# Kernel tuning notes

Hardware: AMD Instinct MI355X
Metric: run time of the kernel (lower is better)

Reference implementation:

```python
import jax, jax.numpy as jnp
import numpy as np

SCALE = 2.0 ** 10.5
DROPOUT_P = 0.5


def setup_inputs() -> dict:
    key = jax.random.key(0)
    ks = jax.random.split(key, 8)
    B, G, S, D_IN, D_H = 1, 8, 4096, 3, 8
    return {
        "x1": jax.random.normal(ks[0], (B, G, S, D_IN), dtype=jnp.float32),
        "x2": jax.random.normal(ks[1], (B, G, S, D_IN), dtype=jnp.float32),
        "Wq": jax.random.normal(ks[2], (D_H, D_IN), dtype=jnp.float32),
        "bq": jax.random.normal(ks[3], (D_H,), dtype=jnp.float32),
        "Wk": jax.random.normal(ks[4], (D_H, D_IN), dtype=jnp.float32),
        "bk": jax.random.normal(ks[5], (D_H,), dtype=jnp.float32),
        "Wv": jax.random.normal(ks[6], (D_H, D_IN), dtype=jnp.float32),
        "bv": jax.random.normal(ks[7], (D_H,), dtype=jnp.float32),
    }


def reference(x1, x2, Wq, bq, Wk, bk, Wv, bv):
    # Linear projections (torch Linear: x @ W.T + b)
    q = jnp.einsum("bgsd,hd->bgsh", x1, Wq) + bq  # [B,G,S,8]
    k = jnp.einsum("bgsd,hd->bgsh", x2, Wk) + bk
    v = jnp.einsum("bgsd,hd->bgsh", x1, Wv) + bv
    # scores scaled by custom factor 2**10.5 (multiplied, not divided)
    scores = jnp.einsum("bgsh,bgth->bgst", q, k) * jnp.float32(SCALE)  # [B,G,S,S]
    probs = jax.nn.softmax(scores, axis=-1)
    # dropout p=0.5 (training mode), deterministic mask, inverted scaling
    mask = jax.random.bernoulli(jax.random.key(42), 1.0 - DROPOUT_P, probs.shape)
    probs = jnp.where(mask, probs / jnp.float32(1.0 - DROPOUT_P), jnp.float32(0.0))
    out = jnp.einsum("bgst,bgth->bgsh", probs, v)  # [B,G,S,8]
    return out
```

## Files before the change

kernel.cpp:

```cpp
#include <hip/hip_runtime.h>
#include <stdint.h>

namespace {

constexpr int G = 8;
constexpr int S = 4096;
constexpr int RPB = 64;
constexpr int RPW = 8;
constexpr int NW = 8;
constexpr int LOGCAP = 64;
constexpr float K2C = (float)(1448.15468787004945 * 1.44269504088896340736);
constexpr float CUT = 32.0f;

__device__ __forceinline__ uint32_t rotl32(uint32_t x, uint32_t n) {
  return (x << n) | (x >> (32u - n));
}

__device__ __forceinline__ void tfround(uint32_t& x0, uint32_t& x1, uint32_t r) {
  x0 += x1;
  x1 = rotl32(x1, r);
  x1 ^= x0;
}

__device__ __forceinline__ void threefry2x32(uint32_t c0, uint32_t c1,
                                             uint32_t& r0, uint32_t& r1) {
  const uint32_t ks0 = 0u;
  const uint32_t ks1 = 42u;
  const uint32_t ks2 = 0x1BD11BF0u;
  uint32_t x0 = c0 + ks0;
  uint32_t x1 = c1 + ks1;
  tfround(x0, x1, 13); tfround(x0, x1, 15); tfround(x0, x1, 26); tfround(x0, x1, 6);
  x0 += ks1; x1 += ks2 + 1u;
  tfround(x0, x1, 17); tfround(x0, x1, 29); tfround(x0, x1, 16); tfround(x0, x1, 24);
  x0 += ks2; x1 += ks0 + 2u;
  tfround(x0, x1, 13); tfround(x0, x1, 15); tfround(x0, x1, 26); tfround(x0, x1, 6);
  x0 += ks0; x1 += ks1 + 3u;
  tfround(x0, x1, 17); tfround(x0, x1, 29); tfround(x0, x1, 16); tfround(x0, x1, 24);
  x0 += ks1; x1 += ks2 + 4u;
  tfround(x0, x1, 13); tfround(x0, x1, 15); tfround(x0, x1, 26); tfround(x0, x1, 6);
  x0 += ks2; x1 += ks0 + 5u;
  r0 = x0; r1 = x1;
}

__device__ __forceinline__ bool keep_mask(uint32_t i) {
  uint32_t a, b;
  threefry2x32(0u, i, a, b);
  return (((a ^ b) >> 31) == 0u);
}

__global__ __launch_bounds__(512, 4)
void fused_attn(const float* __restrict__ x1, const float* __restrict__ x2,
                const float* __restrict__ Wq, const float* __restrict__ bq,
                const float* __restrict__ Wk, const float* __restrict__ bk,
                const float* __restrict__ Wv, const float* __restrict__ bv,
                float* __restrict__ out) {
  __shared__ __align__(16) float XS[S];
  __shared__ __align__(16) float YS[S];
  __shared__ __align__(16) float ZS[S];
  __shared__ float4 CKs[RPB];
  __shared__ uint32_t LOGB[NW][LOGCAP * 2];

  const int g = blockIdx.x >> 6;
  const int tile = blockIdx.x & 63;
  const int row0 = tile * RPB;
  const int tid = (int)threadIdx.x;
  const int wave = tid >> 6;
  const int lane = tid & 63;

  const float* x2g = x2 + (size_t)g * S * 3;
  const float* x1g = x1 + (size_t)g * S * 3;

  if (tid < RPB) {
    const float* px = x1g + (size_t)(row0 + tid) * 3;
    const float a0 = px[0], a1 = px[1], a2 = px[2];
    float q[8];
#pragma unroll
    for (int h = 0; h < 8; ++h)
      q[h] = bq[h] + a0 * Wq[h * 3 + 0] + a1 * Wq[h * 3 + 1] + a2 * Wq[h * 3 + 2];
    float t0 = 0.f, t1 = 0.f, t2 = 0.f, t3 = 0.f;
#pragma unroll
    for (int h = 0; h < 8; ++h) {
      t0 += q[h] * Wk[h * 3 + 0];
      t1 += q[h] * Wk[h * 3 + 1];
      t2 += q[h] * Wk[h * 3 + 2];
      t3 += q[h] * bk[h];
    }
    CKs[tid] = make_float4(t0 * K2C, t1 * K2C, t2 * K2C, t3 * K2C);
  }

  {
    const float4* src = (const float4*)x2g;
    float4* X4 = (float4*)XS;
    float4* Y4 = (float4*)YS;
    float4* Z4 = (float4*)ZS;
    float4 tmp[6];
#pragma unroll
    for (int it = 0; it < 2; ++it)
#pragma unroll
      for (int k = 0; k < 3; ++k)
        tmp[it * 3 + k] = src[it * 1536 + tid * 3 + k];
#pragma unroll
    for (int it = 0; it < 2; ++it) {
      const float4 f0 = tmp[it * 3 + 0];
      const float4 f1 = tmp[it * 3 + 1];
      const float4 f2 = tmp[it * 3 + 2];
      const int gi = it * 512 + tid;
      X4[gi] = make_float4(f0.x, f0.w, f1.z, f2.y);
      Y4[gi] = make_float4(f0.y, f1.x, f1.w, f2.z);
      Z4[gi] = make_float4(f0.z, f1.y, f2.x, f2.w);
    }
  }
  __syncthreads();

  const float4* X4 = (const float4*)XS;
  const float4* Y4 = (const float4*)YS;
  const float4* Z4 = (const float4*)ZS;

  float4 CK[RPW];
#pragma unroll
  for (int r = 0; r < RPW; ++r) CK[r] = CKs[wave * RPW + r];

  float m[RPW];
#pragma unroll
  for (int r = 0; r < RPW; ++r) m[r] = -3.0e38f;

#pragma unroll 2
  for (int c = 0; c < S / 4 / 64; ++c) {
    const int i4 = (c << 6) + lane;
    const float4 fx = X4[i4], fy = Y4[i4], fz = Z4[i4];
    const float bxa[4] = {fx.x, fx.y, fx.z, fx.w};
    const float bya[4] = {fy.x, fy.y, fy.z, fy.w};
    const float bza[4] = {fz.x, fz.y, fz.z, fz.w};
#pragma unroll
    for (int e = 0; e < 4; ++e) {
      const float bx = bxa[e], by = bya[e], bz = bza[e];
#pragma unroll
      for (int r = 0; r < RPW; ++r)
        m[r] = fmaxf(m[r], fmaf(CK[r].x, bx,
                     fmaf(CK[r].y, by, fmaf(CK[r].z, bz, CK[r].w))));
    }
  }
#pragma unroll
  for (int msk = 1; msk < 64; msk <<= 1) {
#pragma unroll
    for (int r = 0; r < RPW; ++r) m[r] = fmaxf(m[r], __shfl_xor(m[r], msk, 64));
  }
#pragma unroll
  for (int r = 0; r < RPW; ++r) CK[r].w -= m[r];

  uint32_t* LOG = LOGB[wave];
  int cnt = 0;

#pragma unroll 2
  for (int c = 0; c < S / 4 / 64; ++c) {
    const int i4 = (c << 6) + lane;
    const float4 fx = X4[i4], fy = Y4[i4], fz = Z4[i4];
    const float bxa[4] = {fx.x, fx.y, fx.z, fx.w};
    const float bya[4] = {fy.x, fy.y, fy.z, fy.w};
    const float bza[4] = {fz.x, fz.y, fz.z, fz.w};
#pragma unroll
    for (int e = 0; e < 4; ++e) {
      const float bx = bxa[e], by = bya[e], bz = bza[e];
      float d[RPW];
#pragma unroll
      for (int r = 0; r < RPW; ++r)
        d[r] = fmaf(CK[r].x, bx, fmaf(CK[r].y, by, fmaf(CK[r].z, bz, CK[r].w)));
      const float m01 = fmaxf(fmaxf(d[0], d[1]), fmaxf(d[2], d[3]));
      const float m23 = fmaxf(fmaxf(d[4], d[5]), fmaxf(d[6], d[7]));
      const float mx = fmaxf(m01, m23);
      if (__any(mx > -CUT)) {
        const uint32_t tt = (uint32_t)((i4 << 2) + e);
#pragma unroll
        for (int r = 0; r < RPW; ++r) {
          const bool hit = (d[r] > -CUT);
          const unsigned long long bm = __ballot(hit);
          if (bm) {
            const int pos = cnt + (int)__popcll(bm & ((1ull << lane) - 1ull));
            if (hit && pos < LOGCAP) {
              LOG[pos * 2 + 0] = ((uint32_t)r << 12) | tt;
              LOG[pos * 2 + 1] = __float_as_uint(d[r]);
            }
            cnt += (int)__popcll(bm);
          }
        }
      }
    }
  }
  if (cnt > LOGCAP) cnt = LOGCAP;

  const uint32_t grow0 = (uint32_t)(g * S + row0 + wave * RPW);
  float lr = 0.f, lkp = 0.f, a0 = 0.f, a1 = 0.f, a2 = 0.f;

  for (int base = 0; base < cnt; base += 64) {
    const int idx = base + lane;
    const bool val = (idx < cnt);
    const uint32_t w0 = val ? LOG[idx * 2 + 0] : 0u;
    const float dd = val ? __uint_as_float(LOG[idx * 2 + 1]) : 0.0f;
    const int er = (int)(w0 >> 12);
    const uint32_t et = w0 & 4095u;
    const float pr = val ? exp2f(dd) : 0.0f;
    const bool keep = val && keep_mask(((grow0 + (uint32_t)er) << 12) | et);
    float c0 = 0.f, c1 = 0.f, c2 = 0.f, prk = 0.f;
    if (keep) {
      const float* pa = x1g + 3u * et;
      prk = pr;
      c0 = pr * pa[0]; c1 = pr * pa[1]; c2 = pr * pa[2];
    }
    const int nj = (cnt - base < 64) ? (cnt - base) : 64;
    for (int jj = 0; jj < nj; ++jj) {
      const int rj = __shfl(er, jj, 64);
      const float prj = __shfl(pr, jj, 64);
      const float prkj = __shfl(prk, jj, 64);
      const float c0j = __shfl(c0, jj, 64);
      const float c1j = __shfl(c1, jj, 64);
      const float c2j = __shfl(c2, jj, 64);
      const bool mine = (rj == lane);
      lr += mine ? prj : 0.f;
      lkp += mine ? prkj : 0.f;
      a0 += mine ? c0j : 0.f;
      a1 += mine ? c1j : 0.f;
      a2 += mine ? c2j : 0.f;
    }
  }

  if (lane < RPW) {
    const int srow = row0 + wave * RPW + lane;
    const float sc = 2.0f / lr;
    float o[8];
#pragma unroll
    for (int h = 0; h < 8; ++h)
      o[h] = (bv[h] * lkp + Wv[h * 3 + 0] * a0 + Wv[h * 3 + 1] * a1 +
              Wv[h * 3 + 2] * a2) * sc;
    float4* po = (float4*)(out + (size_t)(g * S + srow) * 8);
    po[0] = make_float4(o[0], o[1], o[2], o[3]);
    po[1] = make_float4(o[4], o[5], o[6], o[7]);
  }
}

}

extern "C" void kernel_launch(void* const* d_in, const int* in_sizes, int n_in,
                              void* d_out, int out_size, void* d_ws, size_t ws_size,
                              hipStream_t stream) {
  (void)in_sizes; (void)n_in; (void)d_ws; (void)ws_size; (void)out_size;
  const float* x1 = (const float*)d_in[0];
  const float* x2 = (const float*)d_in[1];
  const float* Wq = (const float*)d_in[2];
  const float* bq = (const float*)d_in[3];
  const float* Wk = (const float*)d_in[4];
  const float* bk = (const float*)d_in[5];
  const float* Wv = (const float*)d_in[6];
  const float* bv = (const float*)d_in[7];
  float* out = (float*)d_out;

  fused_attn<<<dim3(G * (S / RPB)), dim3(512), 0, stream>>>(
      x1, x2, Wq, bq, Wk, bk, Wv, bv, out);
}
```

Before: 91.02 us.

## Replace full max pass with seeded partial max and online rescaling

Instead of a full pass over all 4096 keys to compute each row's exact max, the kernel seeds the max from the first 512 keys, then logs candidates above a threshold relative to that seed and tracks the true max of logged entries for rescaling during accumulation. This removes one of the two full score sweeps. In exchange, the log capacity grows to 256 entries per wave, stored as uint2. Because the seed max can underestimate the true max, more entries may pass the cutoff and overflow the log, which risks dropped terms. The accumulate loop's selects are also rewritten as FMAs with a 0/1 factor.

```diff
diff --git a/kernel.cpp b/kernel.cpp
--- a/kernel.cpp
+++ b/kernel.cpp
@@ -8,7 +8,8 @@
 constexpr int RPB = 64;
 constexpr int RPW = 8;
 constexpr int NW = 8;
-constexpr int LOGCAP = 64;
+constexpr int LOGCAP = 256;
+constexpr int SEEDC = 2;
 constexpr float K2C = (float)(1448.15468787004945 * 1.44269504088896340736);
 constexpr float CUT = 32.0f;
 
@@ -58,7 +59,7 @@
   __shared__ __align__(16) float YS[S];
   __shared__ __align__(16) float ZS[S];
   __shared__ float4 CKs[RPB];
-  __shared__ uint32_t LOGB[NW][LOGCAP * 2];
+  __shared__ uint2 LOGB[NW][LOGCAP];
 
   const int g = blockIdx.x >> 6;
   const int tile = blockIdx.x & 63;
@@ -123,6 +124,35 @@
   float m[RPW];
 #pragma unroll
   for (int r = 0; r < RPW; ++r) m[r] = -3.0e38f;
+#pragma unroll
+  for (int c = 0; c < SEEDC; ++c) {
+    const int i4 = (c << 6) + lane;
+    const float4 fx = X4[i4], fy = Y4[i4], fz = Z4[i4];
+    const float bxa[4] = {fx.x, fx.y, fx.z, fx.w};
+    const float bya[4] = {fy.x, fy.y, fy.z, fy.w};
+    const float bza[4] = {fz.x, fz.y, fz.z, fz.w};
+#pragma unroll
+    for (int e = 0; e < 4; ++e) {
+      const float bx = bxa[e], by = bya[e], bz = bza[e];
+#pragma unroll
+      for (int r = 0; r < RPW; ++r)
+        m[r] = fmaxf(m[r], fmaf(CK[r].x, bx,
+                     fmaf(CK[r].y, by, fmaf(CK[r].z, bz, CK[r].w))));
+    }
+  }
+#pragma unroll
+  for (int msk = 1; msk < 64; msk <<= 1) {
+#pragma unroll
+    for (int r = 0; r < RPW; ++r) m[r] = fmaxf(m[r], __shfl_xor(m[r], msk, 64));
+  }
+#pragma unroll
+  for (int r = 0; r < RPW; ++r) CK[r].w -= m[r];
+
+  uint2* LOG = LOGB[wave];
+  int cnt = 0;
+  float mt[RPW];
+#pragma unroll
+  for (int r = 0; r < RPW; ++r) mt[r] = 0.0f;
 
 #pragma unroll 2
   for (int c = 0; c < S / 4 / 64; ++c) {
@@ -134,33 +164,6 @@
 #pragma unroll
     for (int e = 0; e < 4; ++e) {
       const float bx = bxa[e], by = bya[e], bz = bza[e];
-#pragma unroll
-      for (int r = 0; r < RPW; ++r)
-        m[r] = fmaxf(m[r], fmaf(CK[r].x, bx,
-                     fmaf(CK[r].y, by, fmaf(CK[r].z, bz, CK[r].w))));
-    }
-  }
-#pragma unroll
-  for (int msk = 1; msk < 64; msk <<= 1) {
-#pragma unroll
-    for (int r = 0; r < RPW; ++r) m[r] = fmaxf(m[r], __shfl_xor(m[r], msk, 64));
-  }
-#pragma unroll
-  for (int r = 0; r < RPW; ++r) CK[r].w -= m[r];
-
-  uint32_t* LOG = LOGB[wave];
-  int cnt = 0;
-
-#pragma unroll 2
-  for (int c = 0; c < S / 4 / 64; ++c) {
-    const int i4 = (c << 6) + lane;
-    const float4 fx = X4[i4], fy = Y4[i4], fz = Z4[i4];
-    const float bxa[4] = {fx.x, fx.y, fx.z, fx.w};
-    const float bya[4] = {fy.x, fy.y, fy.z, fy.w};
-    const float bza[4] = {fz.x, fz.y, fz.z, fz.w};
-#pragma unroll
-    for (int e = 0; e < 4; ++e) {
-      const float bx = bxa[e], by = bya[e], bz = bza[e];
       float d[RPW];
 #pragma unroll
       for (int r = 0; r < RPW; ++r)
@@ -176,9 +179,11 @@
           const unsigned long long bm = __ballot(hit);
           if (bm) {
             const int pos = cnt + (int)__popcll(bm & ((1ull << lane) - 1ull));
-            if (hit && pos < LOGCAP) {
-              LOG[pos * 2 + 0] = ((uint32_t)r << 12) | tt;
-              LOG[pos * 2 + 1] = __float_as_uint(d[r]);
+            if (hit) {
+              mt[r] = fmaxf(mt[r], d[r]);
+              if (pos < LOGCAP)
+                LOG[pos] = make_uint2(((uint32_t)r << 12) | tt,
+                                      __float_as_uint(d[r]));
             }
             cnt += (int)__popcll(bm);
           }
@@ -188,17 +193,26 @@
   }
   if (cnt > LOGCAP) cnt = LOGCAP;
 
+#pragma unroll
+  for (int msk = 1; msk < 64; msk <<= 1) {
+#pragma unroll
+    for (int r = 0; r < RPW; ++r) mt[r] = fmaxf(mt[r], __shfl_xor(mt[r], msk, 64));
+  }
+
   const uint32_t grow0 = (uint32_t)(g * S + row0 + wave * RPW);
   float lr = 0.f, lkp = 0.f, a0 = 0.f, a1 = 0.f, a2 = 0.f;
 
   for (int base = 0; base < cnt; base += 64) {
     const int idx = base + lane;
     const bool val = (idx < cnt);
-    const uint32_t w0 = val ? LOG[idx * 2 + 0] : 0u;
-    const float dd = val ? __uint_as_float(LOG[idx * 2 + 1]) : 0.0f;
-    const int er = (int)(w0 >> 12);
-    const uint32_t et = w0 & 4095u;
-    const float pr = val ? exp2f(dd) : 0.0f;
+    const uint2 w = val ? LOG[idx] : make_uint2(0u, 0u);
+    const int er = (int)(w.x >> 12);
+    const uint32_t et = w.x & 4095u;
+    const float dd = __uint_as_float(w.y);
+    float Mi = mt[0];
+#pragma unroll
+    for (int r = 1; r < RPW; ++r) Mi = (er == r) ? mt[r] : Mi;
+    const float pr = val ? exp2f(dd - Mi) : 0.0f;
     const bool keep = val && keep_mask(((grow0 + (uint32_t)er) << 12) | et);
     float c0 = 0.f, c1 = 0.f, c2 = 0.f, prk = 0.f;
     if (keep) {
@@ -214,12 +228,12 @@
       const float c0j = __shfl(c0, jj, 64);
       const float c1j = __shfl(c1, jj, 64);
       const float c2j = __shfl(c2, jj, 64);
-      const bool mine = (rj == lane);
-      lr += mine ? prj : 0.f;
-      lkp += mine ? prkj : 0.f;
-      a0 += mine ? c0j : 0.f;
-      a1 += mine ? c1j : 0.f;
-      a2 += mine ? c2j : 0.f;
+      const float sel = (rj == lane) ? 1.0f : 0.0f;
+      lr = fmaf(sel, prj, lr);
+      lkp = fmaf(sel, prkj, lkp);
+      a0 = fmaf(sel, c0j, a0);
+      a1 = fmaf(sel, c1j, a1);
+      a2 = fmaf(sel, c2j, a2);
     }
   }
 
```

New measurement: 120.9 us. +32.8%, slower.
